# Kernel tuning notes

Measured on AMD Instinct MI355X. Metric: run time of the kernel, lower is better.

Reference implementation:

```python
import jax, jax.numpy as jnp
import numpy as np

N_NODES, N_EDGES, IN_F = 20000, 320000, 64
H1, H2 = 2, 2          # attn heads per GATv2 layer
D1, D2 = 128, 128      # gnn_size per layer
NM = [128, 128]        # nodemlp hidden sizes
EM = [512, 256]        # edgemlp hidden sizes
OUT_F = 1
NEG_SLOPE = 0.2


def _lin_init(key, fan_in, fan_out):
    kw, kb = jax.random.split(key)
    s = 1.0 / np.sqrt(fan_in)
    return (jax.random.uniform(kw, (fan_in, fan_out), jnp.float32, -s, s),
            jax.random.uniform(kb, (fan_out,), jnp.float32, -s, s))


def setup_inputs() -> dict:
    key = jax.random.key(0)
    ks = jax.random.split(key, 16)
    x = jax.random.normal(ks[0], (N_NODES, IN_F), jnp.float32)
    src = jax.random.randint(ks[1], (N_EDGES,), 0, N_NODES, jnp.int32)
    dst = jax.random.randint(ks[2], (N_EDGES,), 0, N_NODES, jnp.int32)
    # NodeMLP
    nw0, nb0 = _lin_init(ks[3], IN_F, NM[0])
    nw1, nb1 = _lin_init(ks[4], NM[0], NM[1])
    # GATv2 layer 1 (in=IN_F -> H1*D1)
    g1ws, g1bs = _lin_init(ks[5], IN_F, H1 * D1)
    g1wd, g1bd = _lin_init(ks[6], IN_F, H1 * D1)
    g1a = jax.random.normal(ks[7], (H1, D1), jnp.float32) * (1.0 / np.sqrt(D1))
    # GATv2 layer 2 (in=H1*D1 -> H2*D2)
    g2ws, g2bs = _lin_init(ks[8], H1 * D1, H2 * D2)
    g2wd, g2bd = _lin_init(ks[9], H1 * D1, H2 * D2)
    g2a = jax.random.normal(ks[10], (H2, D2), jnp.float32) * (1.0 / np.sqrt(D2))
    # EdgeMLP: in = 2*(NM[-1] + H2*D2) = 768
    e_in = 2 * (NM[-1] + H2 * D2)
    ew0, eb0 = _lin_init(ks[11], e_in, EM[0])
    ew1, eb1 = _lin_init(ks[12], EM[0], EM[1])
    ew2, eb2 = _lin_init(ks[13], EM[1], OUT_F)
    return dict(x=x, src=src, dst=dst,
                nw0=nw0, nb0=nb0, nw1=nw1, nb1=nb1,
                g1ws=g1ws, g1bs=g1bs, g1wd=g1wd, g1bd=g1bd, g1a=g1a,
                g2ws=g2ws, g2bs=g2bs, g2wd=g2wd, g2bd=g2bd, g2a=g2a,
                ew0=ew0, eb0=eb0, ew1=ew1, eb1=eb1, ew2=ew2, eb2=eb2)


def _segment_softmax(logits, dst, n):
    # logits: (E, H); softmax over edges sharing the same dst node
    m = jax.ops.segment_max(logits, dst, num_segments=n)
    e = jnp.exp(logits - m[dst])
    s = jax.ops.segment_sum(e, dst, num_segments=n)
    return e / s[dst]


def _gatv2(h, src, dst, ws, bs, wd, bd, attn, heads, dim, n):
    fs = (h @ ws + bs).reshape(n, heads, dim)   # fc_src
    fd = (h @ wd + bd).reshape(n, heads, dim)   # fc_dst
    e = jax.nn.leaky_relu(fs[src] + fd[dst], NEG_SLOPE)      # (E,H,D)
    logits = jnp.einsum('ehd,hd->eh', e, attn)               # (E,H)
    a = _segment_softmax(logits, dst, n)                      # (E,H)
    out = jax.ops.segment_sum(a[..., None] * fs[src], dst, num_segments=n)
    return jax.nn.relu(out).reshape(n, heads * dim)           # flatten heads


def reference(x, src, dst,
              nw0, nb0, nw1, nb1,
              g1ws, g1bs, g1wd, g1bd, g1a,
              g2ws, g2bs, g2wd, g2bd, g2a,
              ew0, eb0, ew1, eb1, ew2, eb2):
    n = x.shape[0]
    # NodeMLP (dropout=0 -> identity)
    h1 = jax.nn.relu(x @ nw0 + nb0)
    h1 = jax.nn.relu(h1 @ nw1 + nb1)
    # GCN: two GATv2Conv layers with relu activation, heads flattened
    h2 = _gatv2(x, src, dst, g1ws, g1bs, g1wd, g1bd, g1a, H1, D1, n)
    h2 = _gatv2(h2, src, dst, g2ws, g2bs, g2wd, g2bd, g2a, H2, D2, n)
    # EdgeMLP: gather src/dst, concat, MLP (relu before every layer but first)
    h = jnp.concatenate([h1[src], h1[dst], h2[src], h2[dst]], axis=1)  # (E,768)
    h = h @ ew0 + eb0
    h = jax.nn.relu(h) @ ew1 + eb1
    h = jax.nn.relu(h) @ ew2 + eb2
    return h  # (E, 1) edge scores
```

## Files before the change

### kernel.cpp

```cpp
#include <hip/hip_runtime.h>
#include <hip/hip_bf16.h>

constexpr int N_NODES = 20000;
constexpr int N_EDGES = 320000;

typedef _Float16 half8 __attribute__((ext_vector_type(8)));
typedef _Float16 half4 __attribute__((ext_vector_type(4)));
typedef float    f32x16 __attribute__((ext_vector_type(16)));

__device__ __forceinline__ float lrelu(float x) { return x > 0.f ? x : 0.2f * x; }

__global__ void hist_kernel(const int* __restrict__ dst, int* __restrict__ counts) {
    int e = blockIdx.x * 256 + threadIdx.x;
    if (e < N_EDGES) atomicAdd(&counts[dst[e]], 1);
}

__global__ void scan_all_kernel(const int* __restrict__ counts,
                                int* __restrict__ row_off, int* __restrict__ cursor) {
    __shared__ int ps[1024];
    const int t = threadIdx.x;
    const int base = t * 20;
    int loc[20];
    int sum = 0;
#pragma unroll
    for (int i = 0; i < 20; ++i) {
        const int idx = base + i;
        const int v = (idx < N_NODES) ? counts[idx] : 0;
        loc[i] = sum;
        sum += v;
    }
    ps[t] = sum;
    __syncthreads();
    for (int off = 1; off < 1024; off <<= 1) {
        const int v = (t >= off) ? ps[t - off] : 0;
        __syncthreads();
        ps[t] += v;
        __syncthreads();
    }
    const int ex = ps[t] - sum;
#pragma unroll
    for (int i = 0; i < 20; ++i) {
        const int idx = base + i;
        if (idx < N_NODES) {
            row_off[idx] = ex + loc[i];
            cursor[idx]  = ex + loc[i];
        }
    }
    if (t == 0) row_off[N_NODES] = N_EDGES;
}

__global__ void scatter_kernel(const int* __restrict__ src, const int* __restrict__ dst,
                               int* __restrict__ cursor, int* __restrict__ eidx,
                               int* __restrict__ srcs) {
    int e = blockIdx.x * 256 + threadIdx.x;
    if (e < N_EDGES) {
        int p = atomicAdd(&cursor[dst[e]], 1);
        eidx[p] = e;
        srcs[p] = src[e];
    }
}

template <int K, int M>
__device__ __forceinline__ void pack_one(int idx, const float* __restrict__ W,
                                         int r1, int k1, int r2, int joff, int ldw,
                                         _Float16* __restrict__ H,
                                         _Float16* __restrict__ L) {
    const int l  = idx & 63;
    const int t  = (idx >> 6) % (M / 32);
    const int s  = (idx >> 6) / (M / 32);
    const int j  = joff + t * 32 + (l & 31);
    const int kb = s * 16 + (l >> 5) * 8;
    half8 vh, vl;
#pragma unroll
    for (int i = 0; i < 8; ++i) {
        const int k    = kb + i;
        const int rrow = (k < k1) ? (r1 + k) : (r2 + (k - k1));
        const float w  = W[(size_t)rrow * ldw + j];
        const _Float16 h = (_Float16)w;
        vh[i] = h;
        vl[i] = (_Float16)(w - (float)h);
    }
    reinterpret_cast<half8*>(H)[idx] = vh;
    reinterpret_cast<half8*>(L)[idx] = vl;
}

constexpr int OFF_W1  = 0;
constexpr int OFF_G2S = 16384;
constexpr int OFF_G2D = 24576;
constexpr int OFF_SW0 = 32768;
constexpr int OFF_SW1 = 45056;
constexpr int OFF_DW0 = 57344;
constexpr int OFF_DW1 = 69632;
constexpr int OFF_N1  = 81920;
constexpr int OFF_X   = 83968;
constexpr int PACK_TOT = 89088;

struct PackIn {
    const float *ew1, *g1ws, *g1wd, *g2ws, *g2wd, *ew0, *nw0, *nw1;
    _Float16 *H, *L;
};

__global__ void prepack_all_kernel(PackIn a) {
    const int idx = blockIdx.x * 256 + threadIdx.x;
    if (idx >= PACK_TOT) return;
    _Float16* H = a.H;
    _Float16* L = a.L;
    if (idx < OFF_G2S)
        pack_one<512, 256>(idx - OFF_W1, a.ew1, 0, 512, 0, 0, 256,
                           H + OFF_W1 * 8, L + OFF_W1 * 8);
    else if (idx < OFF_G2D)
        pack_one<256, 256>(idx - OFF_G2S, a.g2ws, 0, 256, 0, 0, 256,
                           H + OFF_G2S * 8, L + OFF_G2S * 8);
    else if (idx < OFF_SW0)
        pack_one<256, 256>(idx - OFF_G2D, a.g2wd, 0, 256, 0, 0, 256,
                           H + OFF_G2D * 8, L + OFF_G2D * 8);
    else if (idx < OFF_SW1)
        pack_one<384, 256>(idx - OFF_SW0, a.ew0, 0, 128, 256, 0, 512,
                           H + OFF_SW0 * 8, L + OFF_SW0 * 8);
    else if (idx < OFF_DW0)
        pack_one<384, 256>(idx - OFF_SW1, a.ew0, 0, 128, 256, 256, 512,
                           H + OFF_SW1 * 8, L + OFF_SW1 * 8);
    else if (idx < OFF_DW1)
        pack_one<384, 256>(idx - OFF_DW0, a.ew0, 128, 128, 512, 0, 512,
                           H + OFF_DW0 * 8, L + OFF_DW0 * 8);
    else if (idx < OFF_N1)
        pack_one<384, 256>(idx - OFF_DW1, a.ew0, 128, 128, 512, 256, 512,
                           H + OFF_DW1 * 8, L + OFF_DW1 * 8);
    else if (idx < OFF_X)
        pack_one<128, 128>(idx - OFF_N1, a.nw1, 0, 128, 0, 0, 128,
                           H + OFF_N1 * 8, L + OFF_N1 * 8);
    else {
        const int xi  = idx - OFF_X;
        const int seg = xi >> 10, r = xi & 1023;
        const int sb  = OFF_X + seg * 1024;
        if (seg == 0)
            pack_one<64, 128>(r, a.nw0, 0, 64, 0, 0, 128, H + sb * 8, L + sb * 8);
        else if (seg <= 2)
            pack_one<64, 128>(r, a.g1ws, 0, 64, 0, (seg - 1) * 128, 256,
                              H + sb * 8, L + sb * 8);
        else
            pack_one<64, 128>(r, a.g1wd, 0, 64, 0, (seg - 3) * 128, 256,
                              H + sb * 8, L + sb * 8);
    }
}

struct LinOut { float* y[6]; const float* b[6]; _Float16* yh[6]; int ldy[6]; int relu[6]; };

template <int K, int TJ, int WR, int K1, int LD1, int LD2, int MINW, int SEG>
__global__ __launch_bounds__(256, MINW) void mfma_linear2_kernel(
    const float* __restrict__ X1, const float* __restrict__ X2,
    const _Float16* __restrict__ BHp, const _Float16* __restrict__ BLp,
    LinOut lo, int N) {
    constexpr int WC    = 4 / WR;
    constexpr int TILES = WC * TJ;
    const int jb  = blockIdx.y;
    const int tid = threadIdx.x;
    const int wv  = tid >> 6, l = tid & 63;
    const int rg  = (WR == 1) ? 0 : ((WR == 4) ? wv : (wv & 1));
    const int cg  = (WR == 1) ? wv : ((WR == 4) ? 0 : (wv >> 1));
    const int m   = l & 31, h = l >> 5;
    const int row = blockIdx.x * (32 * WR) + rg * 32 + m;
    const int ar  = (row < N) ? row : (N - 1);
    const float* __restrict__ xr1 = X1 + (size_t)ar * LD1;
    const float* __restrict__ xr2 = X2 + (size_t)ar * LD2;
    const half8* __restrict__ BH = reinterpret_cast<const half8*>(BHp) + (size_t)jb * SEG;
    const half8* __restrict__ BL = reinterpret_cast<const half8*>(BLp) + (size_t)jb * SEG;
    const float* __restrict__ bp = lo.b[jb];
    float* __restrict__ Y = lo.y[jb];
    _Float16* __restrict__ Yh = lo.yh[jb];
    const int ldy = lo.ldy[jb];
    const int rel = lo.relu[jb];

    f32x16 acc[TJ];
#pragma unroll
    for (int jt = 0; jt < TJ; ++jt) {
        const float bv = bp ? bp[cg * TJ * 32 + jt * 32 + m] : 0.f;
#pragma unroll
        for (int r = 0; r < 16; ++r) acc[jt][r] = bv;
    }

    const int kf = h * 8;
    const float* pf = (kf < K1) ? (xr1 + kf) : (xr2 + (kf - K1));
    float4 xa = *reinterpret_cast<const float4*>(pf);
    float4 xb = *reinterpret_cast<const float4*>(pf + 4);

    for (int s = 0; s < K / 16; ++s) {
        const float xs[8] = {xa.x, xa.y, xa.z, xa.w, xb.x, xb.y, xb.z, xb.w};
        if (s + 1 < K / 16) {
            const int kn = (s + 1) * 16 + h * 8;
            const float* pn = (kn < K1) ? (xr1 + kn) : (xr2 + (kn - K1));
            xa = *reinterpret_cast<const float4*>(pn);
            xb = *reinterpret_cast<const float4*>(pn + 4);
        }
        half8 ah, al;
#pragma unroll
        for (int i = 0; i < 8; ++i) {
            const _Float16 hi = (_Float16)xs[i];
            ah[i] = hi;
            al[i] = (_Float16)(xs[i] - (float)hi);
        }
#pragma unroll
        for (int jt = 0; jt < TJ; ++jt) {
            const int fi = (s * TILES + cg * TJ + jt) * 64 + l;
            const half8 bh = BH[fi];
            const half8 bl = BL[fi];
            acc[jt] = __builtin_amdgcn_mfma_f32_32x32x16_f16(ah, bh, acc[jt], 0, 0, 0);
            acc[jt] = __builtin_amdgcn_mfma_f32_32x32x16_f16(al, bh, acc[jt], 0, 0, 0);
            acc[jt] = __builtin_amdgcn_mfma_f32_32x32x16_f16(ah, bl, acc[jt], 0, 0, 0);
        }
    }

    const int rbase = blockIdx.x * (32 * WR) + rg * 32;
#pragma unroll
    for (int jt = 0; jt < TJ; ++jt) {
        const int j = cg * TJ * 32 + jt * 32 + m;
#pragma unroll
        for (int r = 0; r < 16; ++r) {
            const int orow = rbase + (r & 3) + 8 * (r >> 2) + 4 * h;
            if (orow < N) {
                float v = acc[jt][r];
                if (rel) v = fmaxf(v, 0.f);
                if (Y)  Y[(size_t)orow * ldy + j] = v;
                if (Yh) Yh[(size_t)orow * ldy + j] = (_Float16)v;
            }
        }
    }
}

__global__ void gat_fused_kernel(const _Float16* __restrict__ fsh,
                                 const float* __restrict__ fd,
                                 const float* __restrict__ attn,
                                 const int* __restrict__ row_off,
                                 const int* __restrict__ srcs,
                                 float* __restrict__ outp) {
    const int wv = threadIdx.x >> 6, l = threadIdx.x & 63;
    const int n = blockIdx.x * 4 + wv;
    if (n >= N_NODES) return;
    const int base = (l >> 5) * 128 + (l & 31) * 4;
    const float4 fdv = *reinterpret_cast<const float4*>(&fd[n * 256 + base]);
    const float4 av  = *reinterpret_cast<const float4*>(&attn[base]);
    const int s0 = row_off[n], s1 = row_off[n + 1];

    auto LD = [&](int k) {
        return *reinterpret_cast<const half4*>(&fsh[(size_t)srcs[k] * 256 + base]);
    };
    auto LOGIT = [&](const float4& v) {
        float p = lrelu(v.x + fdv.x) * av.x;
        p = fmaf(lrelu(v.y + fdv.y), av.y, p);
        p = fmaf(lrelu(v.z + fdv.z), av.z, p);
        p = fmaf(lrelu(v.w + fdv.w), av.w, p);
        return p;
    };

    float lsum = 0.f;
    float4 acc = {0.f, 0.f, 0.f, 0.f};
    half4 c0 = {0, 0, 0, 0}, c1 = {0, 0, 0, 0}, n0 = {0, 0, 0, 0}, n1 = {0, 0, 0, 0};
    int i = s0;
    if (i     < s1) c0 = LD(i);
    if (i + 1 < s1) c1 = LD(i + 1);
    if (i + 2 < s1) n0 = LD(i + 2);
    if (i + 3 < s1) n1 = LD(i + 3);
    for (; i + 1 < s1; i += 2) {
        const float4 v0 = {(float)c0.x, (float)c0.y, (float)c0.z, (float)c0.w};
        const float4 v1 = {(float)c1.x, (float)c1.y, (float)c1.z, (float)c1.w};
        c0 = n0; c1 = n1;
        if (i + 4 < s1) n0 = LD(i + 4);
        if (i + 5 < s1) n1 = LD(i + 5);
        float p0 = LOGIT(v0);
        float p1 = LOGIT(v1);
#pragma unroll
        for (int off = 1; off < 32; off <<= 1) {
            p0 += __shfl_xor(p0, off);
            p1 += __shfl_xor(p1, off);
        }
        const float w0 = __expf(p0), w1 = __expf(p1);
        lsum += w0 + w1;
        acc.x = fmaf(w1, v1.x, fmaf(w0, v0.x, acc.x));
        acc.y = fmaf(w1, v1.y, fmaf(w0, v0.y, acc.y));
        acc.z = fmaf(w1, v1.z, fmaf(w0, v0.z, acc.z));
        acc.w = fmaf(w1, v1.w, fmaf(w0, v0.w, acc.w));
    }
    if (i < s1) {
        const float4 v0 = {(float)c0.x, (float)c0.y, (float)c0.z, (float)c0.w};
        float p0 = LOGIT(v0);
#pragma unroll
        for (int off = 1; off < 32; off <<= 1) p0 += __shfl_xor(p0, off);
        const float w0 = __expf(p0);
        lsum += w0;
        acc.x = fmaf(w0, v0.x, acc.x);
        acc.y = fmaf(w0, v0.y, acc.y);
        acc.z = fmaf(w0, v0.z, acc.z);
        acc.w = fmaf(w0, v0.w, acc.w);
    }
    const float inv = (s1 > s0) ? 1.f / lsum : 0.f;
    float4 o;
    o.x = fmaxf(acc.x * inv, 0.f);
    o.y = fmaxf(acc.y * inv, 0.f);
    o.z = fmaxf(acc.z * inv, 0.f);
    o.w = fmaxf(acc.w * inv, 0.f);
    *reinterpret_cast<float4*>(&outp[n * 256 + base]) = o;
}

__global__ __launch_bounds__(256, 2) void edge_mlp7_kernel(
    const _Float16* __restrict__ S, const _Float16* __restrict__ Dn,
    const int* __restrict__ srcs, const int* __restrict__ eidx,
    const int* __restrict__ dstf,
    const _Float16* __restrict__ WpH,
    const float* __restrict__ b1, const float* __restrict__ w2,
    const float* __restrict__ b2, float* __restrict__ out) {
    __shared__ __align__(16) _Float16 Bs[2][8][512];
    const int tid = threadIdx.x;
    const int wv  = tid >> 6, l = tid & 63;
    const int m   = l & 31, h = l >> 5;
    const int e0  = blockIdx.x * 128;
    const int slot = e0 + wv * 32 + m;
    const _Float16* __restrict__ Srow = S  + (size_t)srcs[slot] * 512;
    const _Float16* __restrict__ Drow = Dn + (size_t)dstf[eidx[slot]] * 512;

    f32x16 acc[8];
#pragma unroll
    for (int jt = 0; jt < 8; ++jt) {
        const float bv = b1[jt * 32 + m];
#pragma unroll
        for (int r = 0; r < 16; ++r) acc[jt][r] = bv;
    }

#pragma unroll
    for (int c = 0; c < 2; ++c) {
        const int jt = wv * 2 + c;
        *reinterpret_cast<float4*>(&Bs[0][jt][l * 8]) =
            *reinterpret_cast<const float4*>(WpH + ((size_t)jt * 64 + l) * 8);
    }
    half8 sv = *reinterpret_cast<const half8*>(Srow + h * 8);
    half8 dv = *reinterpret_cast<const half8*>(Drow + h * 8);
    __syncthreads();

    for (int s = 0; s < 32; ++s) {
        const int buf = s & 1;
        float4 bst[2];
        if (s < 31) {
#pragma unroll
            for (int c = 0; c < 2; ++c) {
                const int jt = wv * 2 + c;
                bst[c] = *reinterpret_cast<const float4*>(
                    WpH + ((size_t)((s + 1) * 8 + jt) * 64 + l) * 8);
            }
        }
        half8 xh;
#pragma unroll
        for (int i = 0; i < 8; ++i) {
            const _Float16 t = sv[i] + dv[i];
            xh[i] = t > (_Float16)0.f ? t : (_Float16)0.f;
        }
        if (s < 31) {
            const int ko = (s + 1) * 16 + h * 8;
            sv = *reinterpret_cast<const half8*>(Srow + ko);
            dv = *reinterpret_cast<const half8*>(Drow + ko);
        }
#pragma unroll
        for (int jt = 0; jt < 8; ++jt) {
            const half8 bh = *reinterpret_cast<const half8*>(&Bs[buf][jt][l * 8]);
            acc[jt] = __builtin_amdgcn_mfma_f32_32x32x16_f16(xh, bh, acc[jt], 0, 0, 0);
        }
        if (s < 31) {
#pragma unroll
            for (int c = 0; c < 2; ++c) {
                const int jt = wv * 2 + c;
                *reinterpret_cast<float4*>(&Bs[buf ^ 1][jt][l * 8]) = bst[c];
            }
        }
        __syncthreads();
    }

    float part[16];
#pragma unroll
    for (int r = 0; r < 16; ++r) part[r] = 0.f;
#pragma unroll
    for (int jt = 0; jt < 8; ++jt) {
        const float w2v = w2[jt * 32 + m];
#pragma unroll
        for (int r = 0; r < 16; ++r)
            part[r] = fmaf(fmaxf(acc[jt][r], 0.f), w2v, part[r]);
    }
#pragma unroll
    for (int off = 1; off < 32; off <<= 1)
#pragma unroll
        for (int r = 0; r < 16; ++r) part[r] += __shfl_xor(part[r], off);
    if (m == 0) {
        const float b2v = b2[0];
#pragma unroll
        for (int r = 0; r < 16; ++r) {
            const int row = (r & 3) + 8 * (r >> 2) + 4 * h;
            out[eidx[e0 + wv * 32 + row]] = part[r] + b2v;
        }
    }
}

extern "C" void kernel_launch(void* const* d_in, const int* in_sizes, int n_in,
                              void* d_out, int out_size, void* d_ws, size_t ws_size,
                              hipStream_t stream) {
    (void)in_sizes; (void)n_in; (void)out_size; (void)ws_size;
    const float* x    = (const float*)d_in[0];
    const int*   src  = (const int*)d_in[1];
    const int*   dst  = (const int*)d_in[2];
    const float* nw0  = (const float*)d_in[3];
    const float* nb0  = (const float*)d_in[4];
    const float* nw1  = (const float*)d_in[5];
    const float* nb1  = (const float*)d_in[6];
    const float* g1ws = (const float*)d_in[7];
    const float* g1bs = (const float*)d_in[8];
    const float* g1wd = (const float*)d_in[9];
    const float* g1bd = (const float*)d_in[10];
    const float* g1a  = (const float*)d_in[11];
    const float* g2ws = (const float*)d_in[12];
    const float* g2bs = (const float*)d_in[13];
    const float* g2wd = (const float*)d_in[14];
    const float* g2bd = (const float*)d_in[15];
    const float* g2a  = (const float*)d_in[16];
    const float* ew0  = (const float*)d_in[17];
    const float* eb0  = (const float*)d_in[18];
    const float* ew1  = (const float*)d_in[19];
    const float* eb1  = (const float*)d_in[20];
    const float* ew2  = (const float*)d_in[21];
    const float* eb2  = (const float*)d_in[22];
    float* out = (float*)d_out;

    float* wsF = (float*)d_ws;
    float* h1  = wsF;
    float* g2o = wsF + 2560000;
    float* fsb = wsF + 7680000;
    float* fdb = wsF + 12800000;
    float* g1o = wsF + 17920000;
    _Float16* Sh = (_Float16*)(wsF + 7680000);
    _Float16* Dh = (_Float16*)(wsF + 12800000);
    _Float16* fsh = (_Float16*)(wsF + 23040000);
    int* wsI     = (int*)(wsF + 28160000);
    int* row_off = wsI;
    int* cursor  = wsI + 20016;
    int* eidx    = wsI + 40032;
    int* srcs    = wsI + 360032;
    _Float16* pkH = (_Float16*)((char*)d_ws + 115361280);
    _Float16* pkL = pkH + (size_t)PACK_TOT * 8;

    hipMemsetAsync(cursor, 0, N_NODES * sizeof(int), stream);
    hist_kernel<<<1250, 256, 0, stream>>>(dst, cursor);
    scan_all_kernel<<<1, 1024, 0, stream>>>(cursor, row_off, cursor);
    scatter_kernel<<<1250, 256, 0, stream>>>(src, dst, cursor, eidx, srcs);

    PackIn pin{ew1, g1ws, g1wd, g2ws, g2wd, ew0, nw0, nw1, pkH, pkL};
    prepack_all_kernel<<<(PACK_TOT + 255) / 256, 256, 0, stream>>>(pin);

    {   LinOut lo{};
        lo.y[0] = fsb;        lo.b[0] = nb0;        lo.ldy[0] = 128; lo.relu[0] = 1;
        lo.yh[1] = fsh;       lo.b[1] = g1bs;       lo.ldy[1] = 256;
        lo.yh[2] = fsh + 128; lo.b[2] = g1bs + 128; lo.ldy[2] = 256;
        lo.y[3] = fdb;        lo.b[3] = g1bd;       lo.ldy[3] = 256;
        lo.y[4] = fdb + 128;  lo.b[4] = g1bd + 128; lo.ldy[4] = 256;
        mfma_linear2_kernel<64, 1, 1, 64, 64, 64, 4, 1024>
            <<<dim3(625, 5), 256, 0, stream>>>(x, x, pkH + OFF_X * 8, pkL + OFF_X * 8,
                                               lo, N_NODES); }

    {   LinOut lo{};
        lo.y[0] = h1; lo.b[0] = nb1; lo.ldy[0] = 128; lo.relu[0] = 1;
        mfma_linear2_kernel<128, 1, 1, 128, 128, 128, 4, 0>
            <<<dim3(625, 1), 256, 0, stream>>>(fsb, fsb, pkH + OFF_N1 * 8, pkL + OFF_N1 * 8,
                                               lo, N_NODES); }

    gat_fused_kernel<<<5000, 256, 0, stream>>>(fsh, fdb, g1a, row_off, srcs, g1o);

    {   LinOut lo{};
        lo.yh[0] = fsh; lo.b[0] = g2bs; lo.ldy[0] = 256;
        lo.y[1] = fdb;  lo.b[1] = g2bd; lo.ldy[1] = 256;
        mfma_linear2_kernel<256, 8, 4, 256, 256, 256, 2, 8192>
            <<<dim3(157, 2), 256, 0, stream>>>(g1o, g1o, pkH + OFF_G2S * 8, pkL + OFF_G2S * 8,
                                               lo, N_NODES); }
    gat_fused_kernel<<<5000, 256, 0, stream>>>(fsh, fdb, g2a, row_off, srcs, g2o);

    {   LinOut lo{};
        lo.yh[0] = Sh;       lo.ldy[0] = 512;
        lo.yh[1] = Sh + 256; lo.ldy[1] = 512;
        lo.yh[2] = Dh;       lo.b[2] = eb0;       lo.ldy[2] = 512;
        lo.yh[3] = Dh + 256; lo.b[3] = eb0 + 256; lo.ldy[3] = 512;
        mfma_linear2_kernel<384, 8, 4, 128, 128, 256, 2, 12288>
            <<<dim3(157, 4), 256, 0, stream>>>(h1, g2o, pkH + OFF_SW0 * 8, pkL + OFF_SW0 * 8,
                                               lo, N_NODES); }

    edge_mlp7_kernel<<<N_EDGES / 128, 256, 0, stream>>>(Sh, Dh, srcs, eidx, dst,
                                                        pkH + OFF_W1 * 8,
                                                        eb1, ew2, eb2, out);
}
```

Before: 536.1 us.

## Drop weight low-half split term in node linears and fuse histogram with prepack

Result: faster. 514.7 us (-4.0%).

```diff
diff --git a/kernel.cpp b/kernel.cpp
--- a/kernel.cpp
+++ b/kernel.cpp
@@ -9,11 +9,6 @@
 typedef float    f32x16 __attribute__((ext_vector_type(16)));
 
 __device__ __forceinline__ float lrelu(float x) { return x > 0.f ? x : 0.2f * x; }
-
-__global__ void hist_kernel(const int* __restrict__ dst, int* __restrict__ counts) {
-    int e = blockIdx.x * 256 + threadIdx.x;
-    if (e < N_EDGES) atomicAdd(&counts[dst[e]], 1);
-}
 
 __global__ void scan_all_kernel(const int* __restrict__ counts,
                                 int* __restrict__ row_off, int* __restrict__ cursor) {
@@ -63,25 +58,20 @@
 template <int K, int M>
 __device__ __forceinline__ void pack_one(int idx, const float* __restrict__ W,
                                          int r1, int k1, int r2, int joff, int ldw,
-                                         _Float16* __restrict__ H,
-                                         _Float16* __restrict__ L) {
+                                         _Float16* __restrict__ H) {
     const int l  = idx & 63;
     const int t  = (idx >> 6) % (M / 32);
     const int s  = (idx >> 6) / (M / 32);
     const int j  = joff + t * 32 + (l & 31);
     const int kb = s * 16 + (l >> 5) * 8;
-    half8 vh, vl;
+    half8 vh;
 #pragma unroll
     for (int i = 0; i < 8; ++i) {
         const int k    = kb + i;
         const int rrow = (k < k1) ? (r1 + k) : (r2 + (k - k1));
-        const float w  = W[(size_t)rrow * ldw + j];
-        const _Float16 h = (_Float16)w;
-        vh[i] = h;
-        vl[i] = (_Float16)(w - (float)h);
+        vh[i] = (_Float16)W[(size_t)rrow * ldw + j];
     }
     reinterpret_cast<half8*>(H)[idx] = vh;
-    reinterpret_cast<half8*>(L)[idx] = vl;
 }
 
 constexpr int OFF_W1  = 0;
@@ -94,53 +84,51 @@
 constexpr int OFF_N1  = 81920;
 constexpr int OFF_X   = 83968;
 constexpr int PACK_TOT = 89088;
+constexpr int PACK_BLK = (PACK_TOT + 255) / 256;
+constexpr int HIST_BLK = 1250;
 
 struct PackIn {
     const float *ew1, *g1ws, *g1wd, *g2ws, *g2wd, *ew0, *nw0, *nw1;
-    _Float16 *H, *L;
+    _Float16 *H;
+    const int* dst;
+    int* counts;
 };
 
-__global__ void prepack_all_kernel(PackIn a) {
-    const int idx = blockIdx.x * 256 + threadIdx.x;
+__global__ void hist_prepack_kernel(PackIn a) {
+    if (blockIdx.x < HIST_BLK) {
+        const int e = blockIdx.x * 256 + threadIdx.x;
+        if (e < N_EDGES) atomicAdd(&a.counts[a.dst[e]], 1);
+        return;
+    }
+    const int idx = (blockIdx.x - HIST_BLK) * 256 + threadIdx.x;
     if (idx >= PACK_TOT) return;
     _Float16* H = a.H;
-    _Float16* L = a.L;
     if (idx < OFF_G2S)
-        pack_one<512, 256>(idx - OFF_W1, a.ew1, 0, 512, 0, 0, 256,
-                           H + OFF_W1 * 8, L + OFF_W1 * 8);
+        pack_one<512, 256>(idx - OFF_W1, a.ew1, 0, 512, 0, 0, 256, H + OFF_W1 * 8);
     else if (idx < OFF_G2D)
-        pack_one<256, 256>(idx - OFF_G2S, a.g2ws, 0, 256, 0, 0, 256,
-                           H + OFF_G2S * 8, L + OFF_G2S * 8);
+        pack_one<256, 256>(idx - OFF_G2S, a.g2ws, 0, 256, 0, 0, 256, H + OFF_G2S * 8);
     else if (idx < OFF_SW0)
-        pack_one<256, 256>(idx - OFF_G2D, a.g2wd, 0, 256, 0, 0, 256,
-                           H + OFF_G2D * 8, L + OFF_G2D * 8);
+        pack_one<256, 256>(idx - OFF_G2D, a.g2wd, 0, 256, 0, 0, 256, H + OFF_G2D * 8);
     else if (idx < OFF_SW1)
-        pack_one<384, 256>(idx - OFF_SW0, a.ew0, 0, 128, 256, 0, 512,
-                           H + OFF_SW0 * 8, L + OFF_SW0 * 8);
+        pack_one<384, 256>(idx - OFF_SW0, a.ew0, 0, 128, 256, 0, 512, H + OFF_SW0 * 8);
     else if (idx < OFF_DW0)
-        pack_one<384, 256>(idx - OFF_SW1, a.ew0, 0, 128, 256, 256, 512,
-                           H + OFF_SW1 * 8, L + OFF_SW1 * 8);
+        pack_one<384, 256>(idx - OFF_SW1, a.ew0, 0, 128, 256, 256, 512, H + OFF_SW1 * 8);
     else if (idx < OFF_DW1)
-        pack_one<384, 256>(idx - OFF_DW0, a.ew0, 128, 128, 512, 0, 512,
-                           H + OFF_DW0 * 8, L + OFF_DW0 * 8);
+        pack_one<384, 256>(idx - OFF_DW0, a.ew0, 128, 128, 512, 0, 512, H + OFF_DW0 * 8);
     else if (idx < OFF_N1)
-        pack_one<384, 256>(idx - OFF_DW1, a.ew0, 128, 128, 512, 256, 512,
-                           H + OFF_DW1 * 8, L + OFF_DW1 * 8);
+        pack_one<384, 256>(idx - OFF_DW1, a.ew0, 128, 128, 512, 256, 512, H + OFF_DW1 * 8);
     else if (idx < OFF_X)
-        pack_one<128, 128>(idx - OFF_N1, a.nw1, 0, 128, 0, 0, 128,
-                           H + OFF_N1 * 8, L + OFF_N1 * 8);
+        pack_one<128, 128>(idx - OFF_N1, a.nw1, 0, 128, 0, 0, 128, H + OFF_N1 * 8);
     else {
         const int xi  = idx - OFF_X;
         const int seg = xi >> 10, r = xi & 1023;
         const int sb  = OFF_X + seg * 1024;
         if (seg == 0)
-            pack_one<64, 128>(r, a.nw0, 0, 64, 0, 0, 128, H + sb * 8, L + sb * 8);
+            pack_one<64, 128>(r, a.nw0, 0, 64, 0, 0, 128, H + sb * 8);
         else if (seg <= 2)
-            pack_one<64, 128>(r, a.g1ws, 0, 64, 0, (seg - 1) * 128, 256,
-                              H + sb * 8, L + sb * 8);
+            pack_one<64, 128>(r, a.g1ws, 0, 64, 0, (seg - 1) * 128, 256, H + sb * 8);
         else
-            pack_one<64, 128>(r, a.g1wd, 0, 64, 0, (seg - 3) * 128, 256,
-                              H + sb * 8, L + sb * 8);
+            pack_one<64, 128>(r, a.g1wd, 0, 64, 0, (seg - 3) * 128, 256, H + sb * 8);
     }
 }
 
@@ -149,7 +137,7 @@
 template <int K, int TJ, int WR, int K1, int LD1, int LD2, int MINW, int SEG>
 __global__ __launch_bounds__(256, MINW) void mfma_linear2_kernel(
     const float* __restrict__ X1, const float* __restrict__ X2,
-    const _Float16* __restrict__ BHp, const _Float16* __restrict__ BLp,
+    const _Float16* __restrict__ BHp,
     LinOut lo, int N) {
     constexpr int WC    = 4 / WR;
     constexpr int TILES = WC * TJ;
@@ -164,7 +152,6 @@
     const float* __restrict__ xr1 = X1 + (size_t)ar * LD1;
     const float* __restrict__ xr2 = X2 + (size_t)ar * LD2;
     const half8* __restrict__ BH = reinterpret_cast<const half8*>(BHp) + (size_t)jb * SEG;
-    const half8* __restrict__ BL = reinterpret_cast<const half8*>(BLp) + (size_t)jb * SEG;
     const float* __restrict__ bp = lo.b[jb];
     float* __restrict__ Y = lo.y[jb];
     _Float16* __restrict__ Yh = lo.yh[jb];
@@ -203,10 +190,8 @@
         for (int jt = 0; jt < TJ; ++jt) {
             const int fi = (s * TILES + cg * TJ + jt) * 64 + l;
             const half8 bh = BH[fi];
-            const half8 bl = BL[fi];
             acc[jt] = __builtin_amdgcn_mfma_f32_32x32x16_f16(ah, bh, acc[jt], 0, 0, 0);
             acc[jt] = __builtin_amdgcn_mfma_f32_32x32x16_f16(al, bh, acc[jt], 0, 0, 0);
-            acc[jt] = __builtin_amdgcn_mfma_f32_32x32x16_f16(ah, bl, acc[jt], 0, 0, 0);
         }
     }
 
@@ -440,15 +425,12 @@
     int* eidx    = wsI + 40032;
     int* srcs    = wsI + 360032;
     _Float16* pkH = (_Float16*)((char*)d_ws + 115361280);
-    _Float16* pkL = pkH + (size_t)PACK_TOT * 8;
 
     hipMemsetAsync(cursor, 0, N_NODES * sizeof(int), stream);
-    hist_kernel<<<1250, 256, 0, stream>>>(dst, cursor);
+    PackIn pin{ew1, g1ws, g1wd, g2ws, g2wd, ew0, nw0, nw1, pkH, dst, cursor};
+    hist_prepack_kernel<<<HIST_BLK + PACK_BLK, 256, 0, stream>>>(pin);
     scan_all_kernel<<<1, 1024, 0, stream>>>(cursor, row_off, cursor);
     scatter_kernel<<<1250, 256, 0, stream>>>(src, dst, cursor, eidx, srcs);
-
-    PackIn pin{ew1, g1ws, g1wd, g2ws, g2wd, ew0, nw0, nw1, pkH, pkL};
-    prepack_all_kernel<<<(PACK_TOT + 255) / 256, 256, 0, stream>>>(pin);
 
     {   LinOut lo{};
         lo.y[0] = fsb;        lo.b[0] = nb0;        lo.ldy[0] = 128; lo.relu[0] = 1;
@@ -457,14 +439,12 @@
         lo.y[3] = fdb;        lo.b[3] = g1bd;       lo.ldy[3] = 256;
         lo.y[4] = fdb + 128;  lo.b[4] = g1bd + 128; lo.ldy[4] = 256;
         mfma_linear2_kernel<64, 1, 1, 64, 64, 64, 4, 1024>
-            <<<dim3(625, 5), 256, 0, stream>>>(x, x, pkH + OFF_X * 8, pkL + OFF_X * 8,
-                                               lo, N_NODES); }
+            <<<dim3(625, 5), 256, 0, stream>>>(x, x, pkH + OFF_X * 8, lo, N_NODES); }
 
     {   LinOut lo{};
         lo.y[0] = h1; lo.b[0] = nb1; lo.ldy[0] = 128; lo.relu[0] = 1;
         mfma_linear2_kernel<128, 1, 1, 128, 128, 128, 4, 0>
-            <<<dim3(625, 1), 256, 0, stream>>>(fsb, fsb, pkH + OFF_N1 * 8, pkL + OFF_N1 * 8,
-                                               lo, N_NODES); }
+            <<<dim3(625, 1), 256, 0, stream>>>(fsb, fsb, pkH + OFF_N1 * 8, lo, N_NODES); }
 
     gat_fused_kernel<<<5000, 256, 0, stream>>>(fsh, fdb, g1a, row_off, srcs, g1o);
 
@@ -472,8 +452,7 @@
         lo.yh[0] = fsh; lo.b[0] = g2bs; lo.ldy[0] = 256;
         lo.y[1] = fdb;  lo.b[1] = g2bd; lo.ldy[1] = 256;
         mfma_linear2_kernel<256, 8, 4, 256, 256, 256, 2, 8192>
-            <<<dim3(157, 2), 256, 0, stream>>>(g1o, g1o, pkH + OFF_G2S * 8, pkL + OFF_G2S * 8,
-                                               lo, N_NODES); }
+            <<<dim3(157, 2), 256, 0, stream>>>(g1o, g1o, pkH + OFF_G2S * 8, lo, N_NODES); }
     gat_fused_kernel<<<5000, 256, 0, stream>>>(fsh, fdb, g2a, row_off, srcs, g2o);
 
     {   LinOut lo{};
@@ -482,8 +461,7 @@
         lo.yh[2] = Dh;       lo.b[2] = eb0;       lo.ldy[2] = 512;
         lo.yh[3] = Dh + 256; lo.b[3] = eb0 + 256; lo.ldy[3] = 512;
         mfma_linear2_kernel<384, 8, 4, 128, 128, 256, 2, 12288>
-            <<<dim3(157, 4), 256, 0, stream>>>(h1, g2o, pkH + OFF_SW0 * 8, pkL + OFF_SW0 * 8,
-                                               lo, N_NODES); }
+            <<<dim3(157, 4), 256, 0, stream>>>(h1, g2o, pkH + OFF_SW0 * 8, lo, N_NODES); }
 
     edge_mlp7_kernel<<<N_EDGES / 128, 256, 0, stream>>>(Sh, Dh, srcs, eidx, dst,
                                                         pkH + OFF_W1 * 8,
```
